# Optimization experiments

Measured on AMD Instinct MI355X. Metric: run time of the kernel, lower is better.

The kernel has to match this reference:

```python
import jax, jax.numpy as jnp
import numpy as np

B, S = 1, 4096
H, KV, D, HID = 8, 4, 256, 2304   # heads, kv heads, head_dim, hidden_size
G = H // KV                        # GQA group size
WINDOW = 1024                      # sliding window
THETA = 10000.0                    # rope_local_base_freq (sliding attention)
EPS = 1e-6
SCALE = 256.0 ** -0.5              # query_pre_attn_scalar ** -0.5


def rms_norm(x, w, eps=EPS):
    # Gemma3RMSNorm: fp32 rms over last dim, scale by (1 + weight)
    v = jnp.mean(jnp.square(x), axis=-1, keepdims=True)
    return x * jax.lax.rsqrt(v + eps) * (1.0 + w)


def rope(x, position_ids):
    # x: [B, S, N, D]; split-half rotation as in Gemma3RotaryEmbedding
    d = x.shape[-1]
    inv_freq = 1.0 / (THETA ** (jnp.arange(0, d, 2, dtype=jnp.float32) / d))  # [D/2]
    freqs = position_ids.astype(jnp.float32)[:, :, None] * inv_freq  # [B, S, D/2]
    cos = jnp.cos(freqs)[:, :, None, :]  # [B, S, 1, D/2]
    sin = jnp.sin(freqs)[:, :, None, :]
    x1, x2 = jnp.split(x, 2, axis=-1)
    return jnp.concatenate([x1 * cos - x2 * sin, x1 * sin + x2 * cos], axis=-1)


def setup_inputs() -> dict:
    key = jax.random.key(0)
    ks = jax.random.split(key, 6)
    n = lambda k, shp, sc: jax.random.normal(k, shp, dtype=jnp.float32) * sc
    return {
        "x": n(ks[0], (B, S, HID), 1.0),
        "position_ids": jnp.broadcast_to(jnp.arange(S, dtype=jnp.int32)[None, :], (B, S)),
        "wq": n(ks[1], (HID, H * D), 0.02),
        "wk": n(ks[2], (HID, KV * D), 0.02),
        "wv": n(ks[3], (HID, KV * D), 0.02),
        "wo": n(ks[4], (H * D, HID), 0.02),
        "q_norm_w": jnp.zeros((D,), dtype=jnp.float32),
        "k_norm_w": jnp.zeros((D,), dtype=jnp.float32),
    }


def reference(x, position_ids, wq, wk, wv, wo, q_norm_w, k_norm_w):
    b, s, _ = x.shape
    q = (x @ wq).reshape(b, s, H, D)
    k = (x @ wk).reshape(b, s, KV, D)
    v = (x @ wv).reshape(b, s, KV, D)

    # QK-RMSNorm over head_dim, then RoPE, then query scaling
    q = rms_norm(q, q_norm_w)
    k = rms_norm(k, k_norm_w)
    q = rope(q, position_ids)
    k = rope(k, position_ids)
    q = q * SCALE

    # GQA: group queries over shared KV heads. qg: [B, S, KV, G, D]
    qg = q.reshape(b, s, KV, G, D)
    scores = jnp.einsum('bqcgd,btcd->bcgqt', qg, k)  # [B, KV, G, S, S]

    # causal + sliding-window mask: t <= q and q - t < WINDOW
    pi = position_ids[:, :, None]  # query positions [B, S, 1]
    pj = position_ids[:, None, :]  # key positions   [B, 1, S]
    mask = (pj <= pi) & (pi - pj < WINDOW)  # [B, S, S]
    neg = jnp.finfo(scores.dtype).min
    scores = jnp.where(mask[:, None, None, :, :], scores, neg)

    probs = jax.nn.softmax(scores, axis=-1)
    out = jnp.einsum('bcgqt,btcd->bqcgd', probs, v).reshape(b, s, H * D)
    return out @ wo
```

## Files before the change

### kernel.cpp

```cpp
#include <hip/hip_runtime.h>
#include <stdint.h>

typedef unsigned short u16;
typedef __attribute__((ext_vector_type(8))) short bf16x8;
typedef __attribute__((ext_vector_type(4))) float f32x4;

#define S_LEN 4096
#define HID_DIM 2304
#define QKV_N 4096
#define AO_N 2048
#define HD 256
#define WIN 1024
#define QSCALE 0.0625f

static __device__ __forceinline__ u16 f2bf(float f) {
  union { float f; uint32_t u; } v; v.f = f;
  return (u16)((v.u + 0x7FFFu + ((v.u >> 16) & 1u)) >> 16);
}
static __device__ __forceinline__ float bf2f(u16 h) {
  union { uint32_t u; float f; } v; v.u = ((uint32_t)h) << 16;
  return v.f;
}

static __device__ __forceinline__ void gld16(const void* src, void* dst) {
  __builtin_amdgcn_global_load_lds((const __attribute__((address_space(1))) void*)src,
                                   (__attribute__((address_space(3))) void*)dst, 16, 0, 0);
}

#define BAR() __builtin_amdgcn_s_barrier()
#define LG0() asm volatile("s_waitcnt lgkmcnt(0)" ::: "memory")
#define VM6() asm volatile("s_waitcnt vmcnt(6)" ::: "memory")
#define VM5() asm volatile("s_waitcnt vmcnt(5)" ::: "memory")
#define VM4() asm volatile("s_waitcnt vmcnt(4)" ::: "memory")
#define VM3() asm volatile("s_waitcnt vmcnt(3)" ::: "memory")
#define VM2() asm volatile("s_waitcnt vmcnt(2)" ::: "memory")
#define VM0() asm volatile("s_waitcnt vmcnt(0)" ::: "memory")
#define PRIO1() __builtin_amdgcn_s_setprio(1)
#define PRIO0() __builtin_amdgcn_s_setprio(0)

__global__ __launch_bounds__(256) void k_cvt_bf16(const float* __restrict__ in,
                                                  u16* __restrict__ out, int n) {
  int i = (blockIdx.x * 256 + threadIdx.x) * 4;
  if (i >= n) return;
  float4 v = *(const float4*)(in + i);
  uint64_t p = (uint64_t)f2bf(v.x) | ((uint64_t)f2bf(v.y) << 16)
             | ((uint64_t)f2bf(v.z) << 32) | ((uint64_t)f2bf(v.w) << 48);
  *(uint64_t*)(out + i) = p;
}

__global__ __launch_bounds__(256) void k_sincos(const int* __restrict__ pos_ids,
                                                float* __restrict__ ctab,
                                                float* __restrict__ stab) {
  int idx = blockIdx.x * 256 + threadIdx.x;
  int s = idx >> 7, j = idx & 127;
  float ang = (float)pos_ids[s] * exp2f((float)j * (-13.287712379549449f / 128.0f));
  float sn, c;
  sincosf(ang, &sn, &c);
  ctab[idx] = c;
  stab[idx] = sn;
}

__global__ __launch_bounds__(256) void k_transpose_cvt(const float* __restrict__ in, int C,
                                                       u16* __restrict__ out, int out_stride,
                                                       int row_off) {
  __shared__ float tile[32][33];
  int c0 = blockIdx.x * 32, r0 = blockIdx.y * 32;
  int tx = threadIdx.x & 31, ty = threadIdx.x >> 5;
#pragma unroll
  for (int i = 0; i < 4; i++)
    tile[ty + i * 8][tx] = in[(size_t)(r0 + ty + i * 8) * C + c0 + tx];
  __syncthreads();
#pragma unroll
  for (int i = 0; i < 4; i++)
    out[(size_t)(row_off + c0 + ty + i * 8) * out_stride + r0 + tx] = f2bf(tile[tx][ty + i * 8]);
}

__global__ __launch_bounds__(256) void k_transpose_w(const float* __restrict__ wq,
                                                     const float* __restrict__ wk,
                                                     const float* __restrict__ wv,
                                                     u16* __restrict__ out) {
  int ct = blockIdx.x;
  int r0 = blockIdx.y * 32;
  const float* src;
  int C, c0;
  if (ct < 64) {
    src = wq; C = 2048; c0 = ct * 32;
  } else if (ct < 96) {
    src = wk; C = 1024; c0 = (ct - 64) * 32;
  } else {
    src = wv; C = 1024; c0 = (ct - 96) * 32;
  }
  __shared__ float tile[32][33];
  int tx = threadIdx.x & 31, ty = threadIdx.x >> 5;
#pragma unroll
  for (int i = 0; i < 4; i++)
    tile[ty + i * 8][tx] = src[(size_t)(r0 + ty + i * 8) * C + c0 + tx];
  __syncthreads();
#pragma unroll
  for (int i = 0; i < 4; i++)
    out[(size_t)(ct * 32 + ty + i * 8) * HID_DIM + r0 + tx] = f2bf(tile[tx][ty + i * 8]);
}

template <int MODE>
__global__ __launch_bounds__(512, 2) void k_gemm8p(const u16* __restrict__ A,
                                                   const u16* __restrict__ Bt,
                                                   void* __restrict__ Cout,
                                                   int M, int N, int K,
                                                   const float* __restrict__ ctab,
                                                   const float* __restrict__ stab,
                                                   const float* __restrict__ qnw,
                                                   const float* __restrict__ knw,
                                                   u16* __restrict__ vtb) {
  __shared__ u16 sAB[4 * 256 * 64];
  const int t = threadIdx.x, lane = t & 63, wave = t >> 6;
  const int wr = wave >> 2, wc = wave & 3;
  const int l15 = lane & 15, l4 = lane >> 4;
  const int nbn = N >> 8;
  int bm, bn;
  {
    const int xcd = (int)blockIdx.x & 7, loc = (int)blockIdx.x >> 3;
    if (nbn == 16) {
      bm = (xcd >> 1) * 4 + (loc >> 3);
      bn = (xcd & 1) * 8 + (loc & 7);
    } else {
      const int cpx = gridDim.x >> 3;
      const int wg = xcd * cpx + loc;
      bm = wg / nbn;
      bn = wg % nbn;
    }
  }
  const int NT = K >> 6;
  const int srow = lane >> 3;
  const int sslot = ((lane & 7) ^ srow) * 8;
  const u16* Abase = A + (size_t)(bm * 256) * K;
  const u16* Bbase = Bt + (size_t)(bn * 256) * K;
  f32x4 acc[8][4] = {};
  bf16x8 aF[4][2], b01[2][2], b23[2][2];

#define SA_(b) (&sAB[(b) * 16384])
#define SB_(b) (&sAB[32768 + (b) * 16384])
#define STG_A(BUF, HALF, KT) do {                                                 \
    _Pragma("unroll")                                                             \
    for (int c_ = 0; c_ < 2; c_++) {                                              \
      int rb_ = (HALF) * 128 + (wave * 2 + c_) * 8;                               \
      gld16(Abase + (size_t)(rb_ + srow) * K + ((KT) << 6) + sslot,               \
            SA_(BUF) + rb_ * 64);                                                 \
    }                                                                             \
  } while (0)
#define STG_B(BUF, HALF, KT) do {                                                 \
    _Pragma("unroll")                                                             \
    for (int c_ = 0; c_ < 2; c_++) {                                              \
      int rb_ = (HALF) * 128 + (wave * 2 + c_) * 8;                               \
      gld16(Bbase + (size_t)(rb_ + srow) * K + ((KT) << 6) + sslot,               \
            SB_(BUF) + rb_ * 64);                                                 \
    }                                                                             \
  } while (0)
#define LDA(BUF, M_, KK)                                                          \
  (*(const bf16x8*)&SA_(BUF)[((M_) * 32 + wr * 16 + l15) * 64 +                   \
                             ((((KK) << 2) + l4) ^ (l15 & 7)) * 8])
#define LDB(BUF, N_, KK)                                                          \
  (*(const bf16x8*)&SB_(BUF)[((N_) * 64 + wc * 16 + l15) * 64 +                   \
                             ((((KK) << 2) + l4) ^ (l15 & 7)) * 8])

#define P1_LOADS(b_) do {                                                         \
    _Pragma("unroll") for (int m_ = 0; m_ < 4; m_++)                              \
      _Pragma("unroll") for (int k_ = 0; k_ < 2; k_++)                            \
        aF[m_][k_] = LDA(b_, m_, k_);                                             \
    _Pragma("unroll") for (int n_ = 0; n_ < 2; n_++)                              \
      _Pragma("unroll") for (int k_ = 0; k_ < 2; k_++)                            \
        b01[n_][k_] = LDB(b_, n_, k_);                                            \
  } while (0)
#define P2_LOADS(b_) do {                                                         \
    _Pragma("unroll") for (int n_ = 0; n_ < 2; n_++)                              \
      _Pragma("unroll") for (int k_ = 0; k_ < 2; k_++)                            \
        b23[n_][k_] = LDB(b_, n_ + 2, k_);                                        \
  } while (0)
#define P3_LOADS(b_) do {                                                         \
    _Pragma("unroll") for (int m_ = 0; m_ < 4; m_++)                              \
      _Pragma("unroll") for (int k_ = 0; k_ < 2; k_++)                            \
        aF[m_][k_] = LDA(b_, m_ + 4, k_);                                         \
  } while (0)
#define MFMA16(MOFF, NOFF, BREG) do {                                             \
    _Pragma("unroll") for (int m_ = 0; m_ < 4; m_++)                              \
      _Pragma("unroll") for (int n_ = 0; n_ < 2; n_++)                            \
        _Pragma("unroll") for (int k_ = 0; k_ < 2; k_++)                          \
          acc[m_ + MOFF][n_ + NOFF] = __builtin_amdgcn_mfma_f32_16x16x32_bf16(    \
              aF[m_][k_], BREG[n_][k_], acc[m_ + MOFF][n_ + NOFF], 0, 0, 0);      \
  } while (0)

  STG_A(0, 0, 0);
  STG_B(0, 0, 0);
  STG_B(0, 1, 0);
  STG_A(0, 1, 0);
  VM4();
  BAR();

  for (int tt = 0; tt < NT - 1; ++tt) {
    const int b = tt & 1, nb = b ^ 1;
    P1_LOADS(b);
    STG_A(nb, 0, tt + 1);
    STG_B(nb, 0, tt + 1);
    BAR(); LG0(); PRIO1(); MFMA16(0, 0, b01); PRIO0();
    VM6();
    BAR();
    P2_LOADS(b);
    STG_B(nb, 1, tt + 1);
    BAR(); LG0(); PRIO1(); MFMA16(0, 2, b23); PRIO0();
    VM6();
    BAR();
    P3_LOADS(b);
    STG_A(nb, 1, tt + 1);
    BAR(); LG0(); PRIO1(); MFMA16(4, 0, b01); PRIO0();
    BAR();
    PRIO1(); MFMA16(4, 2, b23); PRIO0();
    VM4();
    BAR();
  }
  {
    const int b = (NT - 1) & 1;
    P1_LOADS(b);
    BAR(); LG0(); PRIO1(); MFMA16(0, 0, b01); PRIO0();
    VM2();
    BAR();
    P2_LOADS(b);
    BAR(); LG0(); PRIO1(); MFMA16(0, 2, b23); PRIO0();
    VM0();
    BAR();
    P3_LOADS(b);
    BAR(); LG0(); PRIO1(); MFMA16(4, 0, b01); PRIO0();
    BAR();
    PRIO1(); MFMA16(4, 2, b23); PRIO0();
  }

  if (MODE == 1) {
    __syncthreads();
    float* slab = (float*)sAB;
    if (bn < 12) {
      const float* wvec = (bn < 8) ? qnw : knw;
      const float scl = (bn < 8) ? QSCALE : 1.0f;
      f32x4 wv4 = *(const f32x4*)&wvec[lane * 4];
#pragma unroll
      for (int mp = 0; mp < 4; mp++) {
#pragma unroll
        for (int mh = 0; mh < 2; mh++) {
          int m = mp * 2 + mh;
#pragma unroll
          for (int n = 0; n < 4; n++)
#pragma unroll
            for (int r = 0; r < 4; r++)
              slab[(mh * 32 + wr * 16 + l4 * 4 + r) * 264 + n * 64 + wc * 16 + l15] =
                  acc[m][n][r];
        }
        __syncthreads();
#pragma unroll
        for (int rr = 0; rr < 8; rr++) {
          int lrow = wave * 8 + rr;
          int grow = bm * 256 + mp * 64 + lrow;
          f32x4 v = *(const f32x4*)&slab[lrow * 264 + lane * 4];
          float ss = v[0] * v[0] + v[1] * v[1] + v[2] * v[2] + v[3] * v[3];
#pragma unroll
          for (int off = 1; off < 64; off <<= 1) ss += __shfl_xor(ss, off);
          float rms = rsqrtf(ss * (1.0f / 256.0f) + 1e-6f);
          float y[4], yo[4];
#pragma unroll
          for (int j = 0; j < 4; j++) y[j] = v[j] * rms * (1.0f + wv4[j]);
#pragma unroll
          for (int j = 0; j < 4; j++) yo[j] = __shfl_xor(y[j], 32);
          f32x4 cv = *(const f32x4*)&ctab[grow * 128 + (lane & 31) * 4];
          f32x4 sv = *(const f32x4*)&stab[grow * 128 + (lane & 31) * 4];
          uint64_t pk = 0;
#pragma unroll
          for (int j = 0; j < 4; j++) {
            float o = (lane < 32) ? (y[j] * cv[j] - yo[j] * sv[j])
                                  : (yo[j] * sv[j] + y[j] * cv[j]);
            pk |= (uint64_t)f2bf(o * scl) << (16 * j);
          }
          *(uint64_t*)&((u16*)Cout)[(size_t)grow * N + bn * 256 + lane * 4] = pk;
        }
        __syncthreads();
      }
    } else {
      const int kvh = bn - 12;
      const int dcol = wave * 32 + (lane >> 1);
      const int shalf = (lane & 1) * 32;
#pragma unroll
      for (int mp = 0; mp < 4; mp++) {
#pragma unroll
        for (int mh = 0; mh < 2; mh++) {
          int m = mp * 2 + mh;
#pragma unroll
          for (int n = 0; n < 4; n++)
#pragma unroll
            for (int r = 0; r < 4; r++)
              slab[(mh * 32 + wr * 16 + l4 * 4 + r) * 264 + n * 64 + wc * 16 + l15] =
                  acc[m][n][r];
        }
        __syncthreads();
        u16* dst = vtb + (size_t)(kvh * 256 + dcol) * S_LEN + bm * 256 + mp * 64 + shalf;
#pragma unroll
        for (int g = 0; g < 4; g++) {
          u16 tmp[8];
#pragma unroll
          for (int jj = 0; jj < 8; jj++)
            tmp[jj] = f2bf(slab[(shalf + g * 8 + jj) * 264 + dcol]);
          *(bf16x8*)(dst + g * 8) = *(const bf16x8*)tmp;
        }
        __syncthreads();
      }
    }
  } else {
#pragma unroll
    for (int m = 0; m < 8; m++)
#pragma unroll
      for (int n = 0; n < 4; n++)
#pragma unroll
        for (int r = 0; r < 4; r++) {
          size_t row = bm * 256 + m * 32 + wr * 16 + l4 * 4 + r;
          size_t col = bn * 256 + n * 64 + wc * 16 + l15;
          ((float*)Cout)[row * N + col] = acc[m][n][r];
        }
  }
#undef SA_
#undef SB_
#undef STG_A
#undef STG_B
#undef LDA
#undef LDB
#undef P1_LOADS
#undef P2_LOADS
#undef P3_LOADS
#undef MFMA16
}

__global__ __launch_bounds__(512, 2) void k_gemm192(const u16* __restrict__ A,
                                                    const u16* __restrict__ Bt,
                                                    float* __restrict__ Cout,
                                                    int M, int N, int K) {
  __shared__ u16 sA[2][256 * 64];
  __shared__ u16 sB[2][192 * 64];
  const int t = threadIdx.x, lane = t & 63, wave = t >> 6;
  const int wr = wave >> 2, wc = wave & 3;
  const int l15 = lane & 15, l4 = lane >> 4;
  const int xcd = (int)blockIdx.x & 7, loc = (int)blockIdx.x >> 3;
  const int bm = (xcd >> 1) * 4 + loc / 6;
  const int bn = (xcd & 1) * 6 + loc % 6;
  const int NT = K >> 6;
  const int srow = lane >> 3;
  const int sslot = ((lane & 7) ^ srow) * 8;
  const u16* Abase = A + (size_t)(bm * 256) * K;
  const u16* Bbase = Bt + (size_t)(bn * 192) * K;
  f32x4 acc[8][3] = {};
  bf16x8 aF[4][2], b01[2][2], b2[2];

#define GA_STG_A(BUF, HALF, KT) do {                                              \
    _Pragma("unroll")                                                             \
    for (int c_ = 0; c_ < 2; c_++) {                                              \
      int rb_ = (HALF) * 128 + (wave * 2 + c_) * 8;                               \
      gld16(Abase + (size_t)(rb_ + srow) * K + ((KT) << 6) + sslot,               \
            &sA[BUF][rb_ * 64]);                                                  \
    }                                                                             \
  } while (0)
#define GA_STG_BC(BUF, CH, KT) do {                                               \
    int rb_ = (CH) * 64 + wave * 8;                                               \
    gld16(Bbase + (size_t)(rb_ + srow) * K + ((KT) << 6) + sslot,                 \
          &sB[BUF][rb_ * 64]);                                                    \
  } while (0)
#define GA_LDA(BUF, M_, KK)                                                       \
  (*(const bf16x8*)&sA[BUF][((M_) * 32 + wr * 16 + l15) * 64 +                    \
                            ((((KK) << 2) + l4) ^ (l15 & 7)) * 8])
#define GA_LDB(BUF, N_, KK)                                                       \
  (*(const bf16x8*)&sB[BUF][((N_) * 64 + wc * 16 + l15) * 64 +                    \
                            ((((KK) << 2) + l4) ^ (l15 & 7)) * 8])
#define GA_P1_LOADS(b_) do {                                                      \
    _Pragma("unroll") for (int m_ = 0; m_ < 4; m_++)                              \
      _Pragma("unroll") for (int k_ = 0; k_ < 2; k_++)                            \
        aF[m_][k_] = GA_LDA(b_, m_, k_);                                          \
    _Pragma("unroll") for (int n_ = 0; n_ < 2; n_++)                              \
      _Pragma("unroll") for (int k_ = 0; k_ < 2; k_++)                            \
        b01[n_][k_] = GA_LDB(b_, n_, k_);                                         \
  } while (0)
#define GA_P2_LOADS(b_) do {                                                      \
    _Pragma("unroll") for (int k_ = 0; k_ < 2; k_++)                              \
      b2[k_] = GA_LDB(b_, 2, k_);                                                 \
  } while (0)
#define GA_P3_LOADS(b_) do {                                                      \
    _Pragma("unroll") for (int m_ = 0; m_ < 4; m_++)                              \
      _Pragma("unroll") for (int k_ = 0; k_ < 2; k_++)                            \
        aF[m_][k_] = GA_LDA(b_, m_ + 4, k_);                                      \
  } while (0)
#define GA_MFMA_N01(MOFF) do {                                                    \
    _Pragma("unroll") for (int m_ = 0; m_ < 4; m_++)                              \
      _Pragma("unroll") for (int n_ = 0; n_ < 2; n_++)                            \
        _Pragma("unroll") for (int k_ = 0; k_ < 2; k_++)                          \
          acc[m_ + MOFF][n_] = __builtin_amdgcn_mfma_f32_16x16x32_bf16(           \
              aF[m_][k_], b01[n_][k_], acc[m_ + MOFF][n_], 0, 0, 0);              \
  } while (0)
#define GA_MFMA_N2(MOFF) do {                                                     \
    _Pragma("unroll") for (int m_ = 0; m_ < 4; m_++)                              \
      _Pragma("unroll") for (int k_ = 0; k_ < 2; k_++)                            \
        acc[m_ + MOFF][2] = __builtin_amdgcn_mfma_f32_16x16x32_bf16(              \
            aF[m_][k_], b2[k_], acc[m_ + MOFF][2], 0, 0, 0);                      \
  } while (0)

  GA_STG_A(0, 0, 0);
  GA_STG_BC(0, 0, 0);
  GA_STG_BC(0, 1, 0);
  GA_STG_BC(0, 2, 0);
  GA_STG_A(0, 1, 0);
  VM3();
  BAR();

  for (int tt = 0; tt < NT - 1; ++tt) {
    const int b = tt & 1, nb = b ^ 1;
    GA_P1_LOADS(b);
    GA_STG_A(nb, 0, tt + 1);
    GA_STG_BC(nb, 0, tt + 1);
    GA_STG_BC(nb, 1, tt + 1);
    BAR(); LG0(); PRIO1(); GA_MFMA_N01(0); PRIO0();
    VM6();
    BAR();
    GA_P2_LOADS(b);
    GA_STG_BC(nb, 2, tt + 1);
    BAR(); LG0(); PRIO1(); GA_MFMA_N2(0); PRIO0();
    VM5();
    BAR();
    GA_P3_LOADS(b);
    GA_STG_A(nb, 1, tt + 1);
    BAR(); LG0(); PRIO1(); GA_MFMA_N01(4); PRIO0();
    BAR();
    PRIO1(); GA_MFMA_N2(4); PRIO0();
    VM3();
    BAR();
  }
  {
    const int b = (NT - 1) & 1;
    GA_P1_LOADS(b);
    BAR(); LG0(); PRIO1(); GA_MFMA_N01(0); PRIO0();
    VM2();
    BAR();
    GA_P2_LOADS(b);
    BAR(); LG0(); PRIO1(); GA_MFMA_N2(0); PRIO0();
    VM0();
    BAR();
    GA_P3_LOADS(b);
    BAR(); LG0(); PRIO1(); GA_MFMA_N01(4); PRIO0();
    BAR();
    PRIO1(); GA_MFMA_N2(4); PRIO0();
  }

#pragma unroll
  for (int m = 0; m < 8; m++)
#pragma unroll
    for (int n = 0; n < 3; n++)
#pragma unroll
      for (int r = 0; r < 4; r++) {
        size_t row = bm * 256 + m * 32 + wr * 16 + l4 * 4 + r;
        size_t col = bn * 192 + n * 64 + wc * 16 + l15;
        Cout[row * N + col] = acc[m][n][r];
      }
#undef GA_STG_A
#undef GA_STG_BC
#undef GA_LDA
#undef GA_LDB
#undef GA_P1_LOADS
#undef GA_P2_LOADS
#undef GA_P3_LOADS
#undef GA_MFMA_N01
#undef GA_MFMA_N2
}

__global__ __launch_bounds__(512, 2) void k_attn(const u16* __restrict__ qkv,
                                                 const u16* __restrict__ vt,
                                                 const int* __restrict__ pos_ids,
                                                 u16* __restrict__ aout) {
  __shared__ u16 lK[2][64 * 256];
  __shared__ u16 lV[2][256 * 64];
  __shared__ u16 lP[8][16 * 64];
  const int bid = blockIdx.x;
  const int wg = (bid & 7) * 32 + (bid >> 3);
  const int kvh = wg >> 6;
  const int q0 = (wg & 63) * 64;
  const int t = threadIdx.x, lane = t & 63, wave = t >> 6;
  const int l15 = lane & 15, l4 = lane >> 4;
  const int head = kvh * 2 + (wave >> 2);
  const int qw = q0 + (wave & 3) * 16;

  bf16x8 qfr[8];
  {
    const u16* qptr = qkv + (size_t)(qw + l15) * QKV_N + head * HD + l4 * 8;
#pragma unroll
    for (int kc = 0; kc < 8; kc++) qfr[kc] = *(const bf16x8*)(qptr + kc * 32);
  }
  f32x4 acc[16] = {};
  float mrow[4], lrow[4];
#pragma unroll
  for (int r = 0; r < 4; r++) { mrow[r] = -1e30f; lrow[r] = 0.0f; }
  int qi[4];
#pragma unroll
  for (int r = 0; r < 4; r++) qi[r] = pos_ids[qw + l4 * 4 + r];

  const int krw = lane >> 5, kcl = lane & 31;
  const int vrw = lane >> 3, vcl = lane & 7;
  const u16* kgb = qkv + 2048 + kvh * HD;
  const u16* vgb = vt + (size_t)kvh * HD * S_LEN;

  int start = q0 - (WIN - 1);
  if (start < 0) start = 0;
  start &= ~63;

#define STAGE_KV(B, T0) do {                                                          \
    _Pragma("unroll")                                                                 \
    for (int i_ = 0; i_ < 4; i_++) {                                                  \
      int ch_ = wave * 4 + i_;                                                        \
      int kr_ = ch_ * 2 + krw;                                                        \
      gld16(kgb + (size_t)((T0) + kr_) * QKV_N + ((kcl ^ (kr_ & 7)) * 8),             \
            &lK[B][ch_ * 512]);                                                       \
      int vr_ = ch_ * 8 + vrw;                                                        \
      gld16(vgb + (size_t)vr_ * S_LEN + (T0) + ((vcl ^ (vr_ & 7)) * 8),               \
            &lV[B][ch_ * 512]);                                                       \
    }                                                                                 \
  } while (0)

  STAGE_KV(0, start);
  __syncthreads();
  int buf = 0;
  for (int t0 = start; t0 <= q0 + 63; t0 += 64) {
    if (t0 + 64 <= q0 + 63) STAGE_KV(buf ^ 1, t0 + 64);
    int kp[4];
#pragma unroll
    for (int kb = 0; kb < 4; kb++) kp[kb] = pos_ids[t0 + kb * 16 + l15];
    f32x4 sv[4] = {};
    PRIO1();
#pragma unroll
    for (int kb = 0; kb < 4; kb++) {
      const char* krow = (const char*)&lK[buf][(kb * 16 + l15) * 256];
      const int sw = ((kb * 16 + l15) & 7) << 4;
#pragma unroll
      for (int kc = 0; kc < 8; kc++) {
        bf16x8 kf = *(const bf16x8*)(krow + ((kc * 64 + l4 * 16) ^ sw));
        sv[kb] = __builtin_amdgcn_mfma_f32_16x16x32_bf16(qfr[kc], kf, sv[kb], 0, 0, 0);
      }
    }
    PRIO0();
    float sloc[4][4], mx[4];
    float need = 0.0f;
#pragma unroll
    for (int r = 0; r < 4; r++) {
      int pi = qi[r];
#pragma unroll
      for (int kb = 0; kb < 4; kb++)
        sloc[r][kb] = ((kp[kb] <= pi) && (pi - kp[kb] < WIN)) ? sv[kb][r] : -__builtin_inff();
      float m_ = fmaxf(fmaxf(sloc[r][0], sloc[r][1]), fmaxf(sloc[r][2], sloc[r][3]));
#pragma unroll
      for (int off = 1; off < 16; off <<= 1) m_ = fmaxf(m_, __shfl_xor(m_, off));
      mx[r] = m_;
      need = fmaxf(need, m_ - mrow[r]);
    }
    bool resc = __any(need > 8.0f);
    if (resc) {
#pragma unroll
      for (int r = 0; r < 4; r++) {
        float nm = fmaxf(mrow[r], mx[r]);
        float al = __expf(mrow[r] - nm);
        mrow[r] = nm;
        lrow[r] *= al;
#pragma unroll
        for (int nd = 0; nd < 16; nd++) acc[nd][r] *= al;
      }
    }
#pragma unroll
    for (int r = 0; r < 4; r++) {
      float nm = mrow[r];
      float e0 = __expf(sloc[r][0] - nm), e1 = __expf(sloc[r][1] - nm);
      float e2 = __expf(sloc[r][2] - nm), e3 = __expf(sloc[r][3] - nm);
      float sum = (e0 + e1) + (e2 + e3);
#pragma unroll
      for (int off = 1; off < 16; off <<= 1) sum += __shfl_xor(sum, off);
      lrow[r] += sum;
      int q = l4 * 4 + r;
      char* lpw = (char*)&lP[wave][0] + q * 128;
      int swp = (q & 7) << 4;
      *(u16*)(lpw + ((l15 * 2) ^ swp)) = f2bf(e0);
      *(u16*)(lpw + ((32 + l15 * 2) ^ swp)) = f2bf(e1);
      *(u16*)(lpw + ((64 + l15 * 2) ^ swp)) = f2bf(e2);
      *(u16*)(lpw + ((96 + l15 * 2) ^ swp)) = f2bf(e3);
    }
#pragma unroll
    for (int kc2 = 0; kc2 < 2; kc2++) {
      int q = l15;
      bf16x8 pa = *(const bf16x8*)((const char*)&lP[wave][0] + q * 128 +
                                   ((kc2 * 64 + l4 * 16) ^ ((q & 7) << 4)));
      PRIO1();
#pragma unroll
      for (int nd = 0; nd < 16; nd++) {
        int d = nd * 16 + l15;
        bf16x8 vf = *(const bf16x8*)((const char*)&lV[buf][d * 64] +
                                     ((kc2 * 64 + l4 * 16) ^ ((d & 7) << 4)));
        acc[nd] = __builtin_amdgcn_mfma_f32_16x16x32_bf16(pa, vf, acc[nd], 0, 0, 0);
      }
      PRIO0();
    }
    __syncthreads();
    buf ^= 1;
  }
  float rinv[4];
#pragma unroll
  for (int r = 0; r < 4; r++) rinv[r] = 1.0f / lrow[r];
#pragma unroll
  for (int nd = 0; nd < 16; nd++)
#pragma unroll
    for (int r = 0; r < 4; r++) {
      size_t row = qw + l4 * 4 + r;
      aout[row * AO_N + head * HD + nd * 16 + l15] = f2bf(acc[nd][r] * rinv[r]);
    }
#undef STAGE_KV
}

extern "C" void kernel_launch(void* const* d_in, const int* in_sizes, int n_in,
                              void* d_out, int out_size, void* d_ws, size_t ws_size,
                              hipStream_t stream) {
  const float* x = (const float*)d_in[0];
  const int* pos = (const int*)d_in[1];
  const float* wq = (const float*)d_in[2];
  const float* wk = (const float*)d_in[3];
  const float* wv = (const float*)d_in[4];
  const float* wo = (const float*)d_in[5];
  const float* qnw = (const float*)d_in[6];
  const float* knw = (const float*)d_in[7];

  u16* qkv = (u16*)d_out;
  float* ctab = (float*)((char*)d_out + 33554432);
  float* stab = (float*)((char*)d_out + 35651584);
  u16* xbf = (u16*)d_ws;
  u16* wT = (u16*)((char*)d_ws + 18874368);
  u16* vtb = (u16*)((char*)d_ws + 28311552);
  u16* aout = xbf;

  k_cvt_bf16<<<9216, 256, 0, stream>>>(x, xbf, S_LEN * HID_DIM);
  k_sincos<<<2048, 256, 0, stream>>>(pos, ctab, stab);
  k_transpose_w<<<dim3(128, 72), 256, 0, stream>>>(wq, wk, wv, wT);
  k_gemm8p<1><<<dim3(256), 512, 0, stream>>>(xbf, wT, qkv, S_LEN, QKV_N, HID_DIM,
                                             ctab, stab, qnw, knw, vtb);
  k_transpose_cvt<<<dim3(72, 64), 256, 0, stream>>>(wo, HID_DIM, wT, 2048, 0);
  k_attn<<<dim3(256), 512, 0, stream>>>(qkv, vtb, pos, aout);
  k_gemm192<<<dim3(192), 512, 0, stream>>>(aout, wT, (float*)d_out, S_LEN, HID_DIM, 2048);
}
```

Measured before the change: 226.7 us.

## Prefetch two K-tiles ahead in both GEMM kernels with deeper vmcnt waits

```diff
diff --git a/kernel.cpp b/kernel.cpp
--- a/kernel.cpp
+++ b/kernel.cpp
@@ -29,11 +29,8 @@
 
 #define BAR() __builtin_amdgcn_s_barrier()
 #define LG0() asm volatile("s_waitcnt lgkmcnt(0)" ::: "memory")
-#define VM6() asm volatile("s_waitcnt vmcnt(6)" ::: "memory")
-#define VM5() asm volatile("s_waitcnt vmcnt(5)" ::: "memory")
-#define VM4() asm volatile("s_waitcnt vmcnt(4)" ::: "memory")
-#define VM3() asm volatile("s_waitcnt vmcnt(3)" ::: "memory")
-#define VM2() asm volatile("s_waitcnt vmcnt(2)" ::: "memory")
+#define VM8() asm volatile("s_waitcnt vmcnt(8)" ::: "memory")
+#define VM7() asm volatile("s_waitcnt vmcnt(7)" ::: "memory")
 #define VM0() asm volatile("s_waitcnt vmcnt(0)" ::: "memory")
 #define PRIO1() __builtin_amdgcn_s_setprio(1)
 #define PRIO0() __builtin_amdgcn_s_setprio(0)
@@ -192,39 +189,54 @@
   STG_B(0, 0, 0);
   STG_B(0, 1, 0);
   STG_A(0, 1, 0);
-  VM4();
+  STG_A(1, 0, 1);
+  STG_B(1, 0, 1);
+  STG_B(1, 1, 1);
+  STG_A(1, 1, 1);
+  VM8();
   BAR();
 
-  for (int tt = 0; tt < NT - 1; ++tt) {
-    const int b = tt & 1, nb = b ^ 1;
+  for (int tt = 0; tt < NT - 2; ++tt) {
+    const int b = tt & 1;
     P1_LOADS(b);
-    STG_A(nb, 0, tt + 1);
-    STG_B(nb, 0, tt + 1);
     BAR(); LG0(); PRIO1(); MFMA16(0, 0, b01); PRIO0();
-    VM6();
     BAR();
     P2_LOADS(b);
-    STG_B(nb, 1, tt + 1);
+    STG_A(b, 0, tt + 2);
+    STG_B(b, 0, tt + 2);
     BAR(); LG0(); PRIO1(); MFMA16(0, 2, b23); PRIO0();
-    VM6();
     BAR();
     P3_LOADS(b);
-    STG_A(nb, 1, tt + 1);
+    STG_B(b, 1, tt + 2);
     BAR(); LG0(); PRIO1(); MFMA16(4, 0, b01); PRIO0();
     BAR();
+    STG_A(b, 1, tt + 2);
+    BAR(); PRIO1(); MFMA16(4, 2, b23); PRIO0();
+    VM8();
+    BAR();
+  }
+  {
+    const int b = (NT - 2) & 1;
+    P1_LOADS(b);
+    BAR(); LG0(); PRIO1(); MFMA16(0, 0, b01); PRIO0();
+    BAR();
+    P2_LOADS(b);
+    BAR(); LG0(); PRIO1(); MFMA16(0, 2, b23); PRIO0();
+    BAR();
+    P3_LOADS(b);
+    BAR(); LG0(); PRIO1(); MFMA16(4, 0, b01); PRIO0();
+    BAR();
     PRIO1(); MFMA16(4, 2, b23); PRIO0();
-    VM4();
+    VM0();
     BAR();
   }
   {
     const int b = (NT - 1) & 1;
     P1_LOADS(b);
     BAR(); LG0(); PRIO1(); MFMA16(0, 0, b01); PRIO0();
-    VM2();
     BAR();
     P2_LOADS(b);
     BAR(); LG0(); PRIO1(); MFMA16(0, 2, b23); PRIO0();
-    VM0();
     BAR();
     P3_LOADS(b);
     BAR(); LG0(); PRIO1(); MFMA16(4, 0, b01); PRIO0();
@@ -407,40 +419,56 @@
   GA_STG_BC(0, 1, 0);
   GA_STG_BC(0, 2, 0);
   GA_STG_A(0, 1, 0);
-  VM3();
+  GA_STG_A(1, 0, 1);
+  GA_STG_BC(1, 0, 1);
+  GA_STG_BC(1, 1, 1);
+  GA_STG_BC(1, 2, 1);
+  GA_STG_A(1, 1, 1);
+  VM7();
   BAR();
 
-  for (int tt = 0; tt < NT - 1; ++tt) {
-    const int b = tt & 1, nb = b ^ 1;
+  for (int tt = 0; tt < NT - 2; ++tt) {
+    const int b = tt & 1;
     GA_P1_LOADS(b);
-    GA_STG_A(nb, 0, tt + 1);
-    GA_STG_BC(nb, 0, tt + 1);
-    GA_STG_BC(nb, 1, tt + 1);
     BAR(); LG0(); PRIO1(); GA_MFMA_N01(0); PRIO0();
-    VM6();
     BAR();
     GA_P2_LOADS(b);
-    GA_STG_BC(nb, 2, tt + 1);
+    GA_STG_A(b, 0, tt + 2);
+    GA_STG_BC(b, 0, tt + 2);
+    GA_STG_BC(b, 1, tt + 2);
     BAR(); LG0(); PRIO1(); GA_MFMA_N2(0); PRIO0();
-    VM5();
     BAR();
     GA_P3_LOADS(b);
-    GA_STG_A(nb, 1, tt + 1);
+    GA_STG_BC(b, 2, tt + 2);
     BAR(); LG0(); PRIO1(); GA_MFMA_N01(4); PRIO0();
     BAR();
+    GA_STG_A(b, 1, tt + 2);
+    BAR(); PRIO1(); GA_MFMA_N2(4); PRIO0();
+    VM7();
+    BAR();
+  }
+  {
+    const int b = (NT - 2) & 1;
+    GA_P1_LOADS(b);
+    BAR(); LG0(); PRIO1(); GA_MFMA_N01(0); PRIO0();
+    BAR();
+    GA_P2_LOADS(b);
+    BAR(); LG0(); PRIO1(); GA_MFMA_N2(0); PRIO0();
+    BAR();
+    GA_P3_LOADS(b);
+    BAR(); LG0(); PRIO1(); GA_MFMA_N01(4); PRIO0();
+    BAR();
     PRIO1(); GA_MFMA_N2(4); PRIO0();
-    VM3();
+    VM0();
     BAR();
   }
   {
     const int b = (NT - 1) & 1;
     GA_P1_LOADS(b);
     BAR(); LG0(); PRIO1(); GA_MFMA_N01(0); PRIO0();
-    VM2();
     BAR();
     GA_P2_LOADS(b);
     BAR(); LG0(); PRIO1(); GA_MFMA_N2(0); PRIO0();
-    VM0();
     BAR();
     GA_P3_LOADS(b);
     BAR(); LG0(); PRIO1(); GA_MFMA_N01(4); PRIO0();
```

New measurement: 235.8 us. 1.04x slower.

## Compute transposed QK scores to keep P in registers, drop LDS round-trip

Applied to the files above, without the earlier changes.

```diff
diff --git a/kernel.cpp b/kernel.cpp
--- a/kernel.cpp
+++ b/kernel.cpp
@@ -475,7 +475,6 @@
                                                  u16* __restrict__ aout) {
   __shared__ u16 lK[2][64 * 256];
   __shared__ u16 lV[2][256 * 64];
-  __shared__ u16 lP[8][16 * 64];
   const int bid = blockIdx.x;
   const int wg = (bid & 7) * 32 + (bid >> 3);
   const int kvh = wg >> 6;
@@ -492,12 +491,8 @@
     for (int kc = 0; kc < 8; kc++) qfr[kc] = *(const bf16x8*)(qptr + kc * 32);
   }
   f32x4 acc[16] = {};
-  float mrow[4], lrow[4];
-#pragma unroll
-  for (int r = 0; r < 4; r++) { mrow[r] = -1e30f; lrow[r] = 0.0f; }
-  int qi[4];
-#pragma unroll
-  for (int r = 0; r < 4; r++) qi[r] = pos_ids[qw + l4 * 4 + r];
+  float mreg = -1e30f, lreg = 0.0f;
+  const int qpos = qw + l15;
 
   const int krw = lane >> 5, kcl = lane & 31;
   const int vrw = lane >> 3, vcl = lane & 7;
@@ -526,9 +521,6 @@
   int buf = 0;
   for (int t0 = start; t0 <= q0 + 63; t0 += 64) {
     if (t0 + 64 <= q0 + 63) STAGE_KV(buf ^ 1, t0 + 64);
-    int kp[4];
-#pragma unroll
-    for (int kb = 0; kb < 4; kb++) kp[kb] = pos_ids[t0 + kb * 16 + l15];
     f32x4 sv[4] = {};
     PRIO1();
 #pragma unroll
@@ -538,64 +530,78 @@
 #pragma unroll
       for (int kc = 0; kc < 8; kc++) {
         bf16x8 kf = *(const bf16x8*)(krow + ((kc * 64 + l4 * 16) ^ sw));
-        sv[kb] = __builtin_amdgcn_mfma_f32_16x16x32_bf16(qfr[kc], kf, sv[kb], 0, 0, 0);
+        sv[kb] = __builtin_amdgcn_mfma_f32_16x16x32_bf16(kf, qfr[kc], sv[kb], 0, 0, 0);
       }
     }
     PRIO0();
-    float sloc[4][4], mx[4];
-    float need = 0.0f;
-#pragma unroll
-    for (int r = 0; r < 4; r++) {
-      int pi = qi[r];
-#pragma unroll
-      for (int kb = 0; kb < 4; kb++)
-        sloc[r][kb] = ((kp[kb] <= pi) && (pi - kp[kb] < WIN)) ? sv[kb][r] : -__builtin_inff();
-      float m_ = fmaxf(fmaxf(sloc[r][0], sloc[r][1]), fmaxf(sloc[r][2], sloc[r][3]));
-#pragma unroll
-      for (int off = 1; off < 16; off <<= 1) m_ = fmaxf(m_, __shfl_xor(m_, off));
-      mx[r] = m_;
-      need = fmaxf(need, m_ - mrow[r]);
+    float p[4][4];
+    float pmax = -__builtin_inff();
+#pragma unroll
+    for (int kb = 0; kb < 4; kb++)
+#pragma unroll
+      for (int r = 0; r < 4; r++) {
+        int key = t0 + kb * 16 + l4 * 4 + r;
+        bool ok = (key <= qpos) && (qpos - key < WIN);
+        p[kb][r] = ok ? sv[kb][r] : -__builtin_inff();
+        pmax = fmaxf(pmax, p[kb][r]);
+      }
+    pmax = fmaxf(pmax, __shfl_xor(pmax, 16));
+    pmax = fmaxf(pmax, __shfl_xor(pmax, 32));
+    bool resc = __any(pmax - mreg > 8.0f);
+    if (resc) {
+      float nm = fmaxf(mreg, pmax);
+      float al = __expf(mreg - nm);
+      mreg = nm;
+      lreg *= al;
+      float alr[4];
+#pragma unroll
+      for (int r = 0; r < 4; r++) alr[r] = __shfl(al, l4 * 4 + r);
+#pragma unroll
+      for (int nd = 0; nd < 16; nd++)
+#pragma unroll
+        for (int r = 0; r < 4; r++) acc[nd][r] *= alr[r];
     }
-    bool resc = __any(need > 8.0f);
-    if (resc) {
+    float sum = 0.0f;
+#pragma unroll
+    for (int kb = 0; kb < 4; kb++)
 #pragma unroll
       for (int r = 0; r < 4; r++) {
-        float nm = fmaxf(mrow[r], mx[r]);
-        float al = __expf(mrow[r] - nm);
-        mrow[r] = nm;
-        lrow[r] *= al;
-#pragma unroll
-        for (int nd = 0; nd < 16; nd++) acc[nd][r] *= al;
-      }
-    }
-#pragma unroll
-    for (int r = 0; r < 4; r++) {
-      float nm = mrow[r];
-      float e0 = __expf(sloc[r][0] - nm), e1 = __expf(sloc[r][1] - nm);
-      float e2 = __expf(sloc[r][2] - nm), e3 = __expf(sloc[r][3] - nm);
-      float sum = (e0 + e1) + (e2 + e3);
-#pragma unroll
-      for (int off = 1; off < 16; off <<= 1) sum += __shfl_xor(sum, off);
-      lrow[r] += sum;
-      int q = l4 * 4 + r;
-      char* lpw = (char*)&lP[wave][0] + q * 128;
-      int swp = (q & 7) << 4;
-      *(u16*)(lpw + ((l15 * 2) ^ swp)) = f2bf(e0);
-      *(u16*)(lpw + ((32 + l15 * 2) ^ swp)) = f2bf(e1);
-      *(u16*)(lpw + ((64 + l15 * 2) ^ swp)) = f2bf(e2);
-      *(u16*)(lpw + ((96 + l15 * 2) ^ swp)) = f2bf(e3);
-    }
-#pragma unroll
-    for (int kc2 = 0; kc2 < 2; kc2++) {
-      int q = l15;
-      bf16x8 pa = *(const bf16x8*)((const char*)&lP[wave][0] + q * 128 +
-                                   ((kc2 * 64 + l4 * 16) ^ ((q & 7) << 4)));
+        p[kb][r] = __expf(p[kb][r] - mreg);
+        sum += p[kb][r];
+      }
+    sum += __shfl_xor(sum, 16);
+    sum += __shfl_xor(sum, 32);
+    lreg += sum;
+    uint32_t pk[4][2];
+#pragma unroll
+    for (int kb = 0; kb < 4; kb++)
+#pragma unroll
+      for (int h = 0; h < 2; h++)
+        pk[kb][h] = (uint32_t)f2bf(p[kb][2 * h]) |
+                    ((uint32_t)f2bf(p[kb][2 * h + 1]) << 16);
+    const int srcA = 32 * (l4 & 1) + l15;
+    const bool lo = lane < 32;
+#pragma unroll
+    for (int H = 0; H < 2; H++) {
+      uint32_t fr[4];
+      {
+        uint32_t a0 = __shfl(pk[2 * H][0], srcA), b0 = __shfl(pk[2 * H + 1][0], srcA);
+        uint32_t a1 = __shfl(pk[2 * H][1], srcA), b1 = __shfl(pk[2 * H + 1][1], srcA);
+        uint32_t a2 = __shfl(pk[2 * H][0], srcA + 16), b2 = __shfl(pk[2 * H + 1][0], srcA + 16);
+        uint32_t a3 = __shfl(pk[2 * H][1], srcA + 16), b3 = __shfl(pk[2 * H + 1][1], srcA + 16);
+        fr[0] = lo ? a0 : b0;
+        fr[1] = lo ? a1 : b1;
+        fr[2] = lo ? a2 : b2;
+        fr[3] = lo ? a3 : b3;
+      }
+      bf16x8 pa;
+      memcpy(&pa, fr, 16);
       PRIO1();
 #pragma unroll
       for (int nd = 0; nd < 16; nd++) {
         int d = nd * 16 + l15;
         bf16x8 vf = *(const bf16x8*)((const char*)&lV[buf][d * 64] +
-                                     ((kc2 * 64 + l4 * 16) ^ ((d & 7) << 4)));
+                                     ((H * 64 + l4 * 16) ^ ((d & 7) << 4)));
         acc[nd] = __builtin_amdgcn_mfma_f32_16x16x32_bf16(pa, vf, acc[nd], 0, 0, 0);
       }
       PRIO0();
@@ -603,15 +609,16 @@
     __syncthreads();
     buf ^= 1;
   }
-  float rinv[4];
-#pragma unroll
-  for (int r = 0; r < 4; r++) rinv[r] = 1.0f / lrow[r];
+  float rinv = 1.0f / lreg;
+  float rv[4];
+#pragma unroll
+  for (int r = 0; r < 4; r++) rv[r] = __shfl(rinv, l4 * 4 + r);
 #pragma unroll
   for (int nd = 0; nd < 16; nd++)
 #pragma unroll
     for (int r = 0; r < 4; r++) {
       size_t row = qw + l4 * 4 + r;
-      aout[row * AO_N + head * HD + nd * 16 + l15] = f2bf(acc[nd][r] * rinv[r]);
+      aout[row * AO_N + head * HD + nd * 16 + l15] = f2bf(acc[nd][r] * rv[r]);
     }
 #undef STAGE_KV
 }
```

After: 222.7 us. About the same (-1.8%).
